# Kernel optimization log

Measured on AMD Instinct MI355X. Metric: run time of the kernel, lower is better.

The kernel has to match this reference:

```python
import jax, jax.numpy as jnp
import numpy as np

BN_EPS = 1e-5

def setup_inputs() -> dict:
    key = jax.random.key(0)
    ks = jax.random.split(key, 8)
    B, C, O, M, K, NR, NT = 64, 8, 8, 32, 32, 8, 8
    ini = float(np.sqrt(3.0 / O / C))
    def p(k):
        return jax.random.uniform(k, (O, C), jnp.float32, -ini, ini)
    return {
        "A": jax.random.normal(ks[0], (B, C, M, K, NR, NT), jnp.float32),
        "P1": p(ks[1]), "P2": p(ks[2]), "P3": p(ks[3]), "P4": p(ks[4]), "P5": p(ks[5]),
        "Wq": p(ks[6]), "Wk": p(ks[7]),
        "gamma": jnp.ones((O,), jnp.float32),
        "beta": jnp.zeros((O,), jnp.float32),
    }

def reference(A, P1, P2, P3, P4, P5, Wq, Wk, gamma, beta):
    B, C, M, Kd, NR, NT = A.shape
    # Branch 1: per-element channel mix, full tensor
    A1 = jnp.einsum('oc,bcmkrt->bomkrt', P1, A)                    # [B,O,M,K,NR,NT]
    # Branch 2: mean over M (axis 2)
    A2 = jnp.einsum('oc,bckrt->bokrt', P2, A.mean(2))[:, :, None]  # [B,O,1,K,NR,NT]
    # Branch 3: mean over NT (axis 5)
    A3 = jnp.einsum('oc,bcmkr->bomkr', P3, A.mean(5))[..., None]   # [B,O,M,K,NR,1]
    # Branch 4: mean over NR (axis 4)
    A4 = jnp.einsum('oc,bcmkt->bomkt', P4, A.mean(4))[:, :, :, :, None, :]  # [B,O,M,K,1,NT]
    # Attention branch over the K axis, built from mean over NR
    temp = A.mean(4)                                               # [B,C,M,K,NT]
    q = jnp.einsum('oc,bcmkt->bomkt', Wq, temp)
    k = jnp.einsum('oc,bcmkt->bomkt', Wk, temp)
    v = jnp.einsum('oc,bcmkt->bomkt', P5, temp)
    alpha = jnp.tanh(jnp.einsum('bomkt,bomlt->bomkl', q, k) / NT)  # [B,O,M,K,K]
    A5 = (jnp.einsum('bomkl,bomlt->bomkt', alpha, v) / Kd)[:, :, :, :, None, :]
    out = A1 + 0.1 * A2 + 0.1 * A3 + 0.5 * A4 + 2.0 * A5          # [B,O,M,K,NR,NT]
    out = jax.nn.relu(out)
    # BatchNorm1d (training mode, biased var) over all dims except channel O
    mean = out.mean(axis=(0, 2, 3, 4, 5), keepdims=True)
    var = out.var(axis=(0, 2, 3, 4, 5), keepdims=True)
    g = gamma[None, :, None, None, None, None]
    bta = beta[None, :, None, None, None, None]
    return (out - mean) * jax.lax.rsqrt(var + BN_EPS) * g + bta
```

## Files before the change

### kernel.cpp

```cpp
#include <hip/hip_runtime.h>


using u16 = unsigned short;
using u32 = unsigned int;

__device__ __forceinline__ void ld8f(const float* p, float* f) {
  float4 a = *(const float4*)p;
  float4 b = *(const float4*)(p + 4);
  f[0] = a.x; f[1] = a.y; f[2] = a.z; f[3] = a.w;
  f[4] = b.x; f[5] = b.y; f[6] = b.z; f[7] = b.w;
}
__device__ __forceinline__ void st8f(float* p, const float* f) {
  *(float4*)p = make_float4(f[0], f[1], f[2], f[3]);
  *(float4*)(p + 4) = make_float4(f[4], f[5], f[6], f[7]);
}
__device__ __forceinline__ u16 f2b(float f) {
  u32 x = __float_as_uint(f);
  x += 0x7fffu + ((x >> 16) & 1u);
  return (u16)(x >> 16);
}
__device__ __forceinline__ float b2f(u16 h) {
  return __uint_as_float(((u32)h) << 16);
}
__device__ __forceinline__ float fast_tanh(float x) {
  float e = __expf(2.0f * x);
  return 1.0f - 2.0f / (e + 1.0f);
}

__global__ void k1_a2pre(
    const float* __restrict__ A, const float* __restrict__ P2,
    float* __restrict__ a2pre, float* __restrict__ stats) {
  const int b = blockIdx.x >> 3;
  const int kq = blockIdx.x & 7;
  const int tid = threadIdx.x;
  if (blockIdx.x == 0 && tid < 16) stats[tid] = 0.0f;
  const int j = kq * 256 + tid;
  float mc[8];
#pragma unroll
  for (int c = 0; c < 8; ++c) {
    const float* base = A + ((size_t)(b * 8 + c) * 65536 + j);
    float s = 0.0f;
#pragma unroll
    for (int m = 0; m < 32; ++m) s += base[m * 2048];
    mc[c] = s * (1.0f / 32.0f);
  }
#pragma unroll
  for (int o = 0; o < 8; ++o) {
    float a2 = 0.0f;
#pragma unroll
    for (int c = 0; c < 8; ++c) a2 = fmaf(P2[o * 8 + c], mc[c], a2);
    a2pre[(size_t)(b * 8 + o) * 2048 + j] = 0.1f * a2;
  }
}

template <bool BF16OUT>
__global__ __launch_bounds__(256, 2) void k2_main(
    const float* __restrict__ A,
    const float* __restrict__ a2pre,
    const float* __restrict__ P1,
    const float* __restrict__ P3,
    const float* __restrict__ P4,
    const float* __restrict__ P5,
    const float* __restrict__ Wq,
    const float* __restrict__ Wk,
    float* __restrict__ outp,
    u16* __restrict__ xb,
    float* __restrict__ stats) {
  __shared__ float qb[8 * 260];
  __shared__ float kb[8 * 260];
  __shared__ float vb[8 * 260];
  __shared__ float a5b[8 * 260];
  __shared__ float sred[64];

  const int tid = threadIdx.x;
  const int b = blockIdx.x >> 5;
  const int m = blockIdx.x & 31;
  const int k = tid >> 3;
  const int r = tid & 7;

  float acc[8][8];
  float acc3[8];
  float qv[8], kv[8], vv[8];
#pragma unroll
  for (int o = 0; o < 8; ++o) {
    acc3[o] = 0.0f;
#pragma unroll
    for (int t = 0; t < 8; ++t) acc[o][t] = 0.0f;
  }
#pragma unroll
  for (int t = 0; t < 8; ++t) { qv[t] = 0.0f; kv[t] = 0.0f; vv[t] = 0.0f; }

#pragma unroll
  for (int c = 0; c < 8; ++c) {
    float ar[8];
    ld8f(A + ((size_t)((b * 8 + c) * 32 + m) * 2048 + tid * 8), ar);
    float trc[8];
#pragma unroll
    for (int t = 0; t < 8; ++t) {
      float x = ar[t];
      x += __shfl_xor(x, 1, 64);
      x += __shfl_xor(x, 2, 64);
      x += __shfl_xor(x, 4, 64);
      trc[t] = x * 0.125f;
    }
    const float mtc = (ar[0] + ar[1] + ar[2] + ar[3] +
                       ar[4] + ar[5] + ar[6] + ar[7]) * 0.125f;
#pragma unroll
    for (int o = 0; o < 8; ++o) {
      const float w1 = P1[o * 8 + c];
      const float w4 = 0.5f * P4[o * 8 + c];
      acc3[o] = fmaf(0.1f * P3[o * 8 + c], mtc, acc3[o]);
#pragma unroll
      for (int t = 0; t < 8; ++t)
        acc[o][t] = fmaf(w1, ar[t], fmaf(w4, trc[t], acc[o][t]));
    }
    const float wq = Wq[r * 8 + c];
    const float wk = Wk[r * 8 + c];
    const float wv = P5[r * 8 + c];
#pragma unroll
    for (int t = 0; t < 8; ++t) {
      qv[t] = fmaf(wq, trc[t], qv[t]);
      kv[t] = fmaf(wk, trc[t], kv[t]);
      vv[t] = fmaf(wv, trc[t], vv[t]);
    }
  }

#pragma unroll
  for (int o = 0; o < 8; ++o) {
    float a2v[8];
    ld8f(a2pre + ((size_t)(b * 8 + o) * 2048 + tid * 8), a2v);
#pragma unroll
    for (int t = 0; t < 8; ++t) acc[o][t] += a2v[t] + acc3[o];
  }

  st8f(&qb[r * 260 + k * 8], qv);
  st8f(&kb[r * 260 + k * 8], kv);
  st8f(&vb[r * 260 + k * 8], vv);
  __syncthreads();

  {
    const int o = tid >> 5;
    const int kq = (tid >> 2) & 7;
    const int lo = tid & 3;
    float qf[4][8];
#pragma unroll
    for (int kl = 0; kl < 4; ++kl)
      ld8f(&qb[o * 260 + (kq * 4 + kl) * 8], qf[kl]);
    float a5p[4][8];
#pragma unroll
    for (int kl = 0; kl < 4; ++kl)
#pragma unroll
      for (int t = 0; t < 8; ++t) a5p[kl][t] = 0.0f;

#pragma unroll
    for (int ll = 0; ll < 8; ++ll) {
      const int l = lo * 8 + ll;
      float krw[8];
      ld8f(&kb[o * 260 + l * 8], krw);
      float al[4];
#pragma unroll
      for (int kl = 0; kl < 4; ++kl) {
        float s = 0.0f;
#pragma unroll
        for (int t = 0; t < 8; ++t) s = fmaf(qf[kl][t], krw[t], s);
        al[kl] = fast_tanh(s * 0.125f);
      }
      float vrw[8];
      ld8f(&vb[o * 260 + l * 8], vrw);
#pragma unroll
      for (int kl = 0; kl < 4; ++kl)
#pragma unroll
        for (int t = 0; t < 8; ++t)
          a5p[kl][t] = fmaf(al[kl], vrw[t], a5p[kl][t]);
    }
#pragma unroll
    for (int kl = 0; kl < 4; ++kl)
#pragma unroll
      for (int t = 0; t < 8; ++t) {
        float x = a5p[kl][t];
        x += __shfl_xor(x, 1, 64);
        x += __shfl_xor(x, 2, 64);
        a5p[kl][t] = x * 0.0625f;
      }
#pragma unroll
    for (int kl = 0; kl < 4; ++kl) {
      const float w0 = lo == 0 ? a5p[kl][0] : lo == 1 ? a5p[kl][2]
                      : lo == 2 ? a5p[kl][4] : a5p[kl][6];
      const float w1 = lo == 0 ? a5p[kl][1] : lo == 1 ? a5p[kl][3]
                      : lo == 2 ? a5p[kl][5] : a5p[kl][7];
      *(float2*)&a5b[o * 260 + (kq * 4 + kl) * 8 + lo * 2] = make_float2(w0, w1);
    }
  }
  __syncthreads();

  float psum[8], psq[8];
#pragma unroll
  for (int o = 0; o < 8; ++o) { psum[o] = 0.0f; psq[o] = 0.0f; }
  const size_t outbase = (size_t)(b * 256 + m) * 2048 + tid * 8;
#pragma unroll
  for (int o = 0; o < 8; ++o) {
    float a5f[8];
    ld8f(&a5b[o * 260 + k * 8], a5f);
    float x8[8];
#pragma unroll
    for (int t = 0; t < 8; ++t) {
      float x = acc[o][t] + a5f[t];
      x = fmaxf(x, 0.0f);
      psum[o] += x;
      psq[o] = fmaf(x, x, psq[o]);
      x8[t] = x;
    }
    if (BF16OUT) {
      uint4 u;
      u.x = (u32)f2b(x8[0]) | ((u32)f2b(x8[1]) << 16);
      u.y = (u32)f2b(x8[2]) | ((u32)f2b(x8[3]) << 16);
      u.z = (u32)f2b(x8[4]) | ((u32)f2b(x8[5]) << 16);
      u.w = (u32)f2b(x8[6]) | ((u32)f2b(x8[7]) << 16);
      *(uint4*)(xb + (outbase + (size_t)o * 65536)) = u;
    } else {
      st8f(outp + (outbase + (size_t)o * 65536), x8);
    }
  }
#pragma unroll
  for (int o = 0; o < 8; ++o) {
    float s = psum[o], q = psq[o];
#pragma unroll
    for (int mask = 32; mask >= 1; mask >>= 1) {
      s += __shfl_xor(s, mask, 64);
      q += __shfl_xor(q, mask, 64);
    }
    psum[o] = s; psq[o] = q;
  }
  const int lane = tid & 63;
  const int wid = tid >> 6;
  if (lane == 0) {
#pragma unroll
    for (int o = 0; o < 8; ++o) {
      sred[wid * 16 + o * 2] = psum[o];
      sred[wid * 16 + o * 2 + 1] = psq[o];
    }
  }
  __syncthreads();
  if (tid < 16) {
    float s = sred[tid] + sred[16 + tid] + sred[32 + tid] + sred[48 + tid];
    atomicAdd(&stats[tid], s);
  }
}

__global__ void k3_norm_inplace(float* __restrict__ outp,
                                const float* __restrict__ stats,
                                const float* __restrict__ gamma,
                                const float* __restrict__ beta) {
  const int idx = blockIdx.x * 256 + threadIdx.x;
  const size_t e0 = (size_t)idx * 8;
  const int o = (int)(e0 >> 16) & 7;
  const float N = 4194304.0f;
  const float mean = stats[o * 2] / N;
  float var = stats[o * 2 + 1] / N - mean * mean;
  var = fmaxf(var, 0.0f);
  const float inv = rsqrtf(var + 1e-5f);
  const float g = gamma[o] * inv;
  const float sh = beta[o] - mean * g;
  float f[8];
  ld8f(outp + e0, f);
#pragma unroll
  for (int t = 0; t < 8; ++t) f[t] = fmaf(f[t], g, sh);
  st8f(outp + e0, f);
}

__global__ void k3_norm_bf16(const u16* __restrict__ xb,
                             float* __restrict__ outp,
                             const float* __restrict__ stats,
                             const float* __restrict__ gamma,
                             const float* __restrict__ beta) {
  const int idx = blockIdx.x * 256 + threadIdx.x;
  const size_t e0 = (size_t)idx * 8;
  const int o = (int)(e0 >> 16) & 7;
  const float N = 4194304.0f;
  const float mean = stats[o * 2] / N;
  float var = stats[o * 2 + 1] / N - mean * mean;
  var = fmaxf(var, 0.0f);
  const float inv = rsqrtf(var + 1e-5f);
  const float g = gamma[o] * inv;
  const float sh = beta[o] - mean * g;
  const uint4 u = *(const uint4*)(xb + e0);
  float f[8];
  f[0] = b2f((u16)(u.x & 0xffffu)); f[1] = b2f((u16)(u.x >> 16));
  f[2] = b2f((u16)(u.y & 0xffffu)); f[3] = b2f((u16)(u.y >> 16));
  f[4] = b2f((u16)(u.z & 0xffffu)); f[5] = b2f((u16)(u.z >> 16));
  f[6] = b2f((u16)(u.w & 0xffffu)); f[7] = b2f((u16)(u.w >> 16));
#pragma unroll
  for (int t = 0; t < 8; ++t) f[t] = fmaf(f[t], g, sh);
  st8f(outp + e0, f);
}

extern "C" void kernel_launch(void* const* d_in, const int* in_sizes, int n_in,
                              void* d_out, int out_size, void* d_ws, size_t ws_size,
                              hipStream_t stream) {
  const float* A  = (const float*)d_in[0];
  const float* P1 = (const float*)d_in[1];
  const float* P2 = (const float*)d_in[2];
  const float* P3 = (const float*)d_in[3];
  const float* P4 = (const float*)d_in[4];
  const float* P5 = (const float*)d_in[5];
  const float* Wq = (const float*)d_in[6];
  const float* Wk = (const float*)d_in[7];
  const float* gamma = (const float*)d_in[8];
  const float* beta  = (const float*)d_in[9];
  float* outp = (float*)d_out;

  float* stats = (float*)d_ws;
  float* a2pre = (float*)((char*)d_ws + 256);
  u16* xb = (u16*)((char*)d_ws + 256 + (size_t)4 * 1024 * 1024);
  const size_t need_bf16 = 256 + (size_t)4 * 1024 * 1024 + (size_t)67108864;
  const bool use_bf16 = (ws_size >= need_bf16);

  hipLaunchKernelGGL(k1_a2pre, dim3(512), dim3(256), 0, stream, A, P2, a2pre, stats);
  if (use_bf16) {
    hipLaunchKernelGGL((k2_main<true>), dim3(2048), dim3(256), 0, stream,
                       A, a2pre, P1, P3, P4, P5, Wq, Wk, outp, xb, stats);
    hipLaunchKernelGGL(k3_norm_bf16, dim3(16384), dim3(256), 0, stream,
                       xb, outp, stats, gamma, beta);
  } else {
    hipLaunchKernelGGL((k2_main<false>), dim3(2048), dim3(256), 0, stream,
                       A, a2pre, P1, P3, P4, P5, Wq, Wk, outp, xb, stats);
    hipLaunchKernelGGL(k3_norm_inplace, dim3(16384), dim3(256), 0, stream,
                       outp, stats, gamma, beta);
  }
}
```

Measured before the change: 379.8 us.

## Split M-mean kernel, fp16 intermediate with cascaded in-place normalize, nontemporal stores

Splits the A2 precompute into a coalesced vectorized M-mean kernel plus a small channel-mix kernel. Switches the intermediate from bf16 to fp16. Adds a cascade mode that stores fp16 intermediates inside the output buffer and normalizes back-to-front across several launches when workspace is small. Final stores use nontemporal hints. The aim is to cut strided reads and the cost of the intermediate round trip, but fp16 can overflow or lose range, and the change adds extra launches.

New measurement: 389.6 us. 1.03x slower.

```diff
diff --git a/kernel.cpp b/kernel.cpp
--- a/kernel.cpp
+++ b/kernel.cpp
@@ -1,8 +1,12 @@
 #include <hip/hip_runtime.h>
+#include <hip/hip_fp16.h>
 
 
 using u16 = unsigned short;
 using u32 = unsigned int;
+typedef float f32x4 __attribute__((ext_vector_type(4)));
+
+#define NTOT 33554432
 
 __device__ __forceinline__ void ld8f(const float* p, float* f) {
   float4 a = *(const float4*)p;
@@ -14,46 +18,66 @@
   *(float4*)p = make_float4(f[0], f[1], f[2], f[3]);
   *(float4*)(p + 4) = make_float4(f[4], f[5], f[6], f[7]);
 }
-__device__ __forceinline__ u16 f2b(float f) {
-  u32 x = __float_as_uint(f);
-  x += 0x7fffu + ((x >> 16) & 1u);
-  return (u16)(x >> 16);
-}
-__device__ __forceinline__ float b2f(u16 h) {
-  return __uint_as_float(((u32)h) << 16);
+__device__ __forceinline__ void st8f_nt(float* p, const float* f) {
+  f32x4 a = {f[0], f[1], f[2], f[3]};
+  f32x4 b = {f[4], f[5], f[6], f[7]};
+  __builtin_nontemporal_store(a, (f32x4*)p);
+  __builtin_nontemporal_store(b, (f32x4*)(p + 4));
+}
+__device__ __forceinline__ u16 f2h(float f) {
+  __half h = __float2half_rn(f);
+  return *(u16*)&h;
+}
+__device__ __forceinline__ float h2f(u16 x) {
+  __half h = *(__half*)&x;
+  return __half2float(h);
 }
 __device__ __forceinline__ float fast_tanh(float x) {
   float e = __expf(2.0f * x);
   return 1.0f - 2.0f / (e + 1.0f);
 }
 
-__global__ void k1_a2pre(
-    const float* __restrict__ A, const float* __restrict__ P2,
-    float* __restrict__ a2pre, float* __restrict__ stats) {
+__global__ void k1a_mmean(const float* __restrict__ A, float* __restrict__ mcab,
+                          float* __restrict__ stats) {
   const int b = blockIdx.x >> 3;
-  const int kq = blockIdx.x & 7;
+  const int c = blockIdx.x & 7;
   const int tid = threadIdx.x;
   if (blockIdx.x == 0 && tid < 16) stats[tid] = 0.0f;
-  const int j = kq * 256 + tid;
+  const float* base = A + (size_t)(b * 8 + c) * 65536 + tid * 8;
+  float acc[8];
+#pragma unroll
+  for (int t = 0; t < 8; ++t) acc[t] = 0.0f;
+#pragma unroll
+  for (int m = 0; m < 32; ++m) {
+    float ar[8];
+    ld8f(base + m * 2048, ar);
+#pragma unroll
+    for (int t = 0; t < 8; ++t) acc[t] += ar[t];
+  }
+#pragma unroll
+  for (int t = 0; t < 8; ++t) acc[t] *= (1.0f / 32.0f);
+  st8f(mcab + (size_t)(b * 8 + c) * 2048 + tid * 8, acc);
+}
+
+__global__ void k1b_p2(float* __restrict__ mcab, const float* __restrict__ P2) {
+  const int b = blockIdx.x >> 3;
+  const int j = (blockIdx.x & 7) * 256 + threadIdx.x;
   float mc[8];
 #pragma unroll
-  for (int c = 0; c < 8; ++c) {
-    const float* base = A + ((size_t)(b * 8 + c) * 65536 + j);
+  for (int c = 0; c < 8; ++c) mc[c] = mcab[(size_t)(b * 8 + c) * 2048 + j];
+  float a2[8];
+#pragma unroll
+  for (int o = 0; o < 8; ++o) {
     float s = 0.0f;
 #pragma unroll
-    for (int m = 0; m < 32; ++m) s += base[m * 2048];
-    mc[c] = s * (1.0f / 32.0f);
-  }
-#pragma unroll
-  for (int o = 0; o < 8; ++o) {
-    float a2 = 0.0f;
-#pragma unroll
-    for (int c = 0; c < 8; ++c) a2 = fmaf(P2[o * 8 + c], mc[c], a2);
-    a2pre[(size_t)(b * 8 + o) * 2048 + j] = 0.1f * a2;
-  }
-}
-
-template <bool BF16OUT>
+    for (int c = 0; c < 8; ++c) s = fmaf(P2[o * 8 + c], mc[c], s);
+    a2[o] = 0.1f * s;
+  }
+#pragma unroll
+  for (int o = 0; o < 8; ++o) mcab[(size_t)(b * 8 + o) * 2048 + j] = a2[o];
+}
+
+template <int MODE>
 __global__ __launch_bounds__(256, 2) void k2_main(
     const float* __restrict__ A,
     const float* __restrict__ a2pre,
@@ -210,15 +234,22 @@
       psq[o] = fmaf(x, x, psq[o]);
       x8[t] = x;
     }
-    if (BF16OUT) {
+    const size_t idx = outbase + (size_t)o * 65536;
+    if (MODE == 0) {
+      st8f(outp + idx, x8);
+    } else {
       uint4 u;
-      u.x = (u32)f2b(x8[0]) | ((u32)f2b(x8[1]) << 16);
-      u.y = (u32)f2b(x8[2]) | ((u32)f2b(x8[3]) << 16);
-      u.z = (u32)f2b(x8[4]) | ((u32)f2b(x8[5]) << 16);
-      u.w = (u32)f2b(x8[6]) | ((u32)f2b(x8[7]) << 16);
-      *(uint4*)(xb + (outbase + (size_t)o * 65536)) = u;
-    } else {
-      st8f(outp + (outbase + (size_t)o * 65536), x8);
+      u.x = (u32)f2h(x8[0]) | ((u32)f2h(x8[1]) << 16);
+      u.y = (u32)f2h(x8[2]) | ((u32)f2h(x8[3]) << 16);
+      u.z = (u32)f2h(x8[4]) | ((u32)f2h(x8[5]) << 16);
+      u.w = (u32)f2h(x8[6]) | ((u32)f2h(x8[7]) << 16);
+      u16* dst;
+      if (MODE == 1) {
+        dst = xb;
+      } else {
+        dst = (b * 8 + o < 64) ? xb : (u16*)outp;
+      }
+      *(uint4*)(dst + idx) = u;
     }
   }
 #pragma unroll
@@ -245,6 +276,31 @@
     float s = sred[tid] + sred[16 + tid] + sred[32 + tid] + sred[48 + tid];
     atomicAdd(&stats[tid], s);
   }
+}
+
+__global__ void k3_fp16(const u16* __restrict__ src, float* __restrict__ outp,
+                        const float* __restrict__ stats,
+                        const float* __restrict__ gamma,
+                        const float* __restrict__ beta,
+                        const u32 ebase) {
+  const size_t e0 = (size_t)ebase + ((size_t)blockIdx.x * 256 + threadIdx.x) * 8;
+  const int o = (int)(e0 >> 16) & 7;
+  const float inv_n = 1.0f / 4194304.0f;
+  const float mean = stats[o * 2] * inv_n;
+  float var = stats[o * 2 + 1] * inv_n - mean * mean;
+  var = fmaxf(var, 0.0f);
+  const float inv = rsqrtf(var + 1e-5f);
+  const float g = gamma[o] * inv;
+  const float sh = beta[o] - mean * g;
+  const uint4 u = *(const uint4*)(src + e0);
+  float f[8];
+  f[0] = h2f((u16)(u.x & 0xffffu)); f[1] = h2f((u16)(u.x >> 16));
+  f[2] = h2f((u16)(u.y & 0xffffu)); f[3] = h2f((u16)(u.y >> 16));
+  f[4] = h2f((u16)(u.z & 0xffffu)); f[5] = h2f((u16)(u.z >> 16));
+  f[6] = h2f((u16)(u.w & 0xffffu)); f[7] = h2f((u16)(u.w >> 16));
+#pragma unroll
+  for (int t = 0; t < 8; ++t) f[t] = fmaf(f[t], g, sh);
+  st8f_nt(outp + e0, f);
 }
 
 __global__ void k3_norm_inplace(float* __restrict__ outp,
@@ -254,9 +310,9 @@
   const int idx = blockIdx.x * 256 + threadIdx.x;
   const size_t e0 = (size_t)idx * 8;
   const int o = (int)(e0 >> 16) & 7;
-  const float N = 4194304.0f;
-  const float mean = stats[o * 2] / N;
-  float var = stats[o * 2 + 1] / N - mean * mean;
+  const float inv_n = 1.0f / 4194304.0f;
+  const float mean = stats[o * 2] * inv_n;
+  float var = stats[o * 2 + 1] * inv_n - mean * mean;
   var = fmaxf(var, 0.0f);
   const float inv = rsqrtf(var + 1e-5f);
   const float g = gamma[o] * inv;
@@ -265,33 +321,7 @@
   ld8f(outp + e0, f);
 #pragma unroll
   for (int t = 0; t < 8; ++t) f[t] = fmaf(f[t], g, sh);
-  st8f(outp + e0, f);
-}
-
-__global__ void k3_norm_bf16(const u16* __restrict__ xb,
-                             float* __restrict__ outp,
-                             const float* __restrict__ stats,
-                             const float* __restrict__ gamma,
-                             const float* __restrict__ beta) {
-  const int idx = blockIdx.x * 256 + threadIdx.x;
-  const size_t e0 = (size_t)idx * 8;
-  const int o = (int)(e0 >> 16) & 7;
-  const float N = 4194304.0f;
-  const float mean = stats[o * 2] / N;
-  float var = stats[o * 2 + 1] / N - mean * mean;
-  var = fmaxf(var, 0.0f);
-  const float inv = rsqrtf(var + 1e-5f);
-  const float g = gamma[o] * inv;
-  const float sh = beta[o] - mean * g;
-  const uint4 u = *(const uint4*)(xb + e0);
-  float f[8];
-  f[0] = b2f((u16)(u.x & 0xffffu)); f[1] = b2f((u16)(u.x >> 16));
-  f[2] = b2f((u16)(u.y & 0xffffu)); f[3] = b2f((u16)(u.y >> 16));
-  f[4] = b2f((u16)(u.z & 0xffffu)); f[5] = b2f((u16)(u.z >> 16));
-  f[6] = b2f((u16)(u.w & 0xffffu)); f[7] = b2f((u16)(u.w >> 16));
-#pragma unroll
-  for (int t = 0; t < 8; ++t) f[t] = fmaf(f[t], g, sh);
-  st8f(outp + e0, f);
+  st8f_nt(outp + e0, f);
 }
 
 extern "C" void kernel_launch(void* const* d_in, const int* in_sizes, int n_in,
@@ -310,20 +340,33 @@
   float* outp = (float*)d_out;
 
   float* stats = (float*)d_ws;
-  float* a2pre = (float*)((char*)d_ws + 256);
+  float* mcab = (float*)((char*)d_ws + 256);
   u16* xb = (u16*)((char*)d_ws + 256 + (size_t)4 * 1024 * 1024);
-  const size_t need_bf16 = 256 + (size_t)4 * 1024 * 1024 + (size_t)67108864;
-  const bool use_bf16 = (ws_size >= need_bf16);
-
-  hipLaunchKernelGGL(k1_a2pre, dim3(512), dim3(256), 0, stream, A, P2, a2pre, stats);
-  if (use_bf16) {
-    hipLaunchKernelGGL((k2_main<true>), dim3(2048), dim3(256), 0, stream,
-                       A, a2pre, P1, P3, P4, P5, Wq, Wk, outp, xb, stats);
-    hipLaunchKernelGGL(k3_norm_bf16, dim3(16384), dim3(256), 0, stream,
-                       xb, outp, stats, gamma, beta);
+  const size_t need_full = 256 + (size_t)4 * 1024 * 1024 + (size_t)2 * NTOT;
+  const size_t need_casc = 256 + (size_t)4 * 1024 * 1024 + (size_t)2 * (NTOT / 8);
+
+  hipLaunchKernelGGL(k1a_mmean, dim3(512), dim3(256), 0, stream, A, mcab, stats);
+  hipLaunchKernelGGL(k1b_p2, dim3(512), dim3(256), 0, stream, mcab, P2);
+
+  if (ws_size >= need_full) {
+    hipLaunchKernelGGL((k2_main<1>), dim3(2048), dim3(256), 0, stream,
+                       A, mcab, P1, P3, P4, P5, Wq, Wk, outp, xb, stats);
+    hipLaunchKernelGGL(k3_fp16, dim3(16384), dim3(256), 0, stream,
+                       xb, outp, stats, gamma, beta, 0u);
+  } else if (ws_size >= need_casc) {
+    hipLaunchKernelGGL((k2_main<2>), dim3(2048), dim3(256), 0, stream,
+                       A, mcab, P1, P3, P4, P5, Wq, Wk, outp, xb, stats);
+    hipLaunchKernelGGL(k3_fp16, dim3(8192), dim3(256), 0, stream,
+                       (const u16*)outp, outp, stats, gamma, beta, (u32)(NTOT / 2));
+    hipLaunchKernelGGL(k3_fp16, dim3(4096), dim3(256), 0, stream,
+                       (const u16*)outp, outp, stats, gamma, beta, (u32)(NTOT / 4));
+    hipLaunchKernelGGL(k3_fp16, dim3(2048), dim3(256), 0, stream,
+                       (const u16*)outp, outp, stats, gamma, beta, (u32)(NTOT / 8));
+    hipLaunchKernelGGL(k3_fp16, dim3(2048), dim3(256), 0, stream,
+                       xb, outp, stats, gamma, beta, 0u);
   } else {
-    hipLaunchKernelGGL((k2_main<false>), dim3(2048), dim3(256), 0, stream,
-                       A, a2pre, P1, P3, P4, P5, Wq, Wk, outp, xb, stats);
+    hipLaunchKernelGGL((k2_main<0>), dim3(2048), dim3(256), 0, stream,
+                       A, mcab, P1, P3, P4, P5, Wq, Wk, outp, xb, stats);
     hipLaunchKernelGGL(k3_norm_inplace, dim3(16384), dim3(256), 0, stream,
                        outp, stats, gamma, beta);
   }
```
